# Kernel optimization log

Hardware: AMD Instinct MI355X
Metric: run time of the kernel (lower is better)

## Reference

```python
import jax, jax.numpy as jnp
import numpy as np

K = 7        # kernel_size
G = 16       # group_number
STRIDE = 1
BN_EPS = 1e-5


def setup_inputs() -> dict:
    key = jax.random.key(0)
    ks = jax.random.split(key, 3)
    B, C, H, W = 2, 256, 56, 56
    Cr = C // 4  # reduction_ratio = 4
    x = jax.random.normal(ks[0], (B, C, H, W), dtype=jnp.float32)
    w1 = jax.random.normal(ks[1], (Cr, C), dtype=jnp.float32) * (1.0 / np.sqrt(C))
    b1 = jnp.zeros((Cr,), dtype=jnp.float32)
    gamma = jnp.ones((Cr,), dtype=jnp.float32)
    beta = jnp.zeros((Cr,), dtype=jnp.float32)
    w2 = jax.random.normal(ks[2], (K * K * G, Cr), dtype=jnp.float32) * (1.0 / np.sqrt(Cr))
    b2 = jnp.zeros((K * K * G,), dtype=jnp.float32)
    return {"x": x, "w1": w1, "b1": b1, "gamma": gamma, "beta": beta, "w2": w2, "b2": b2}


def _kernel_gen(x, w1, b1, gamma, beta, w2, b2):
    # 1x1 conv -> BatchNorm (training-mode batch stats) -> ReLU -> 1x1 conv
    t = jnp.einsum('oc,bchw->bohw', w1, x) + b1[None, :, None, None]
    mean = t.mean(axis=(0, 2, 3), keepdims=True)
    var = t.var(axis=(0, 2, 3), keepdims=True)
    t = (t - mean) * jax.lax.rsqrt(var + BN_EPS)
    t = t * gamma[None, :, None, None] + beta[None, :, None, None]
    t = jax.nn.relu(t)
    return jnp.einsum('oc,bchw->bohw', w2, t) + b2[None, :, None, None]


def reference(x, w1, b1, gamma, beta, w2, b2):
    B, C, H, W = x.shape
    nh, nw = H // STRIDE, W // STRIDE  # stride == 1 here
    # kernel generation (stride==1 -> no avg_pool)
    k = _kernel_gen(x, w1, b1, gamma, beta, w2, b2)          # (B, K*K*G, nh, nw)
    kernel = k.reshape(B, K * K, nh, nw, G)                   # raw view, as in torch
    # F.unfold with padding=K//2, stride=1 -> layout (B, C*K*K, L), c-major then k
    p = K // 2
    xp = jnp.pad(x, ((0, 0), (0, 0), (p, p), (p, p)))
    patches = jnp.stack(
        [xp[:, :, i:i + nh, j:j + nw] for i in range(K) for j in range(K)],
        axis=2)                                               # (B, C, K*K, nh, nw)
    flat = patches.reshape(B, C * K * K, nh * nw)             # == torch F.unfold
    ip = flat.reshape(B, C // G, K * K, nh, nw, G)            # raw view, as in torch
    out = (kernel[:, None] * ip).sum(axis=2)                  # (B, C//G, nh, nw, G)
    out = out.reshape(B, C, nh, nw)                           # raw view, as in torch
    return out, kernel
```

## Files before the change

kernel.cpp:

```cpp
#include <hip/hip_runtime.h>

#define HW     3136
#define C_IN   256
#define CR     64
#define KKG    784
#define NB     2
#define NPIX   6272
#define NT25   25
#define BN_EPS 1e-5f

__device__ float g_P[4 * CR * NPIX];
__device__ float g_T[CR * NPIX];
__device__ float g_bs[2 * CR * NT25];
__device__ float g_xg[16 * NPIX * 16];
__device__ float g_w2t[CR * KKG];

__global__ __launch_bounds__(256) void k1a_conv1(const float* __restrict__ x,
                                                 const float* __restrict__ w1,
                                                 const float* __restrict__ w2) {
  int bid = blockIdx.x;
  if (bid >= 800) {
    int t = bid - 800;
    int idx = t * 256 + threadIdx.x;
    for (int j = idx; j < CR * KKG; j += 25 * 256) {
      int c = j / KKG, o = j - c * KKG;
      g_w2t[j] = w2[o * CR + c];
    }
    return;
  }
  int kc     = (bid & 7) >> 1;
  int parity = bid & 1;
  int unit   = (bid >> 3) * 2 + parity;
  int o0     = (unit & 7) * 8;
  int pt     = unit >> 3;
  int p      = pt * 256 + threadIdx.x;
  if (p >= NPIX) return;
  int b = p / HW;
  int u = p - b * HW;

  const float* xb = x + ((size_t)(b * C_IN + kc * 64)) * HW + u;
  const float* w  = w1 + kc * 64;

  float acc[8];
#pragma unroll
  for (int i = 0; i < 8; ++i) acc[i] = 0.0f;
#pragma unroll 8
  for (int c = 0; c < 64; ++c) {
    float xv = xb[(size_t)c * HW];
#pragma unroll
    for (int i = 0; i < 8; ++i)
      acc[i] += w[(o0 + i) * C_IN + c] * xv;
  }
  float* pp = g_P + ((size_t)kc * CR + o0) * NPIX + p;
#pragma unroll
  for (int i = 0; i < 8; ++i) pp[(size_t)i * NPIX] = acc[i];
}

__global__ __launch_bounds__(256) void kRT(const float* __restrict__ x,
                                           const float* __restrict__ b1) {
  int p = blockIdx.x * 256 + threadIdx.x;
  if (blockIdx.y < 64) {
    int o = blockIdx.y;
    bool valid = (p < NPIX);
    float v = 0.0f;
    if (valid) {
      v = b1[o]
        + g_P[((size_t)0 * CR + o) * NPIX + p]
        + g_P[((size_t)1 * CR + o) * NPIX + p]
        + g_P[((size_t)2 * CR + o) * NPIX + p]
        + g_P[((size_t)3 * CR + o) * NPIX + p];
      g_T[(size_t)o * NPIX + p] = v;
    }
    float s  = valid ? v : 0.0f;
    float s2 = valid ? v * v : 0.0f;
#pragma unroll
    for (int off = 32; off > 0; off >>= 1) {
      s  += __shfl_down(s, off);
      s2 += __shfl_down(s2, off);
    }
    __shared__ float sd[8];
    int lane = threadIdx.x & 63, wid = threadIdx.x >> 6;
    if (lane == 0) { sd[wid] = s; sd[4 + wid] = s2; }
    __syncthreads();
    if (threadIdx.x == 0) {
      g_bs[o * NT25 + blockIdx.x]             = sd[0] + sd[1] + sd[2] + sd[3];
      g_bs[CR * NT25 + o * NT25 + blockIdx.x] = sd[4] + sd[5] + sd[6] + sd[7];
    }
  } else {
    int d = blockIdx.y - 64;
    if (p >= NPIX) return;
    int b  = (p >= HW) ? 1 : 0;
    int hw = p - b * HW;
    const float* xp = x + ((size_t)(b * C_IN + d)) * HW + hw;
    float r[16];
#pragma unroll
    for (int cg = 0; cg < 16; ++cg)
      r[cg] = xp[(size_t)cg * (16 * HW)];
    float4* dst = (float4*)(g_xg + (((size_t)d * NPIX + p) << 4));
    dst[0] = make_float4(r[0], r[1], r[2], r[3]);
    dst[1] = make_float4(r[4], r[5], r[6], r[7]);
    dst[2] = make_float4(r[8], r[9], r[10], r[11]);
    dst[3] = make_float4(r[12], r[13], r[14], r[15]);
  }
}

__global__ __launch_bounds__(256) void kB_conv2(const float* __restrict__ gamma,
                                                const float* __restrict__ beta,
                                                const float* __restrict__ b2,
                                                float* __restrict__ kout) {
  __shared__ float ssc[CR], ssh[CR];
  if (threadIdx.x < CR) {
    int o = threadIdx.x;
    float S = 0.f, S2 = 0.f;
#pragma unroll
    for (int px = 0; px < NT25; ++px) {
      S  += g_bs[o * NT25 + px];
      S2 += g_bs[CR * NT25 + o * NT25 + px];
    }
    const float invN = 1.0f / (float)NPIX;
    float mean = S * invN;
    float var  = S2 * invN - mean * mean;
    float inv  = rsqrtf(var + BN_EPS);
    float sc   = gamma[o] * inv;
    ssc[o] = sc;
    ssh[o] = beta[o] - mean * sc;
  }
  __syncthreads();

  int l  = blockIdx.x * 256 + threadIdx.x;
  if (l >= HW) return;
  int o0 = blockIdx.y * 16;
  int b  = blockIdx.z;

  float acc[16];
#pragma unroll
  for (int i = 0; i < 16; ++i) acc[i] = b2[o0 + i];

  const float* Tb = g_T + (size_t)b * HW + l;
  const float* wt = g_w2t + o0;
#pragma unroll 4
  for (int c = 0; c < CR; ++c) {
    float tv = Tb[(size_t)c * NPIX];
    tv = fmaxf(tv * ssc[c] + ssh[c], 0.0f);
#pragma unroll
    for (int i = 0; i < 16; ++i)
      acc[i] += wt[c * KKG + i] * tv;
  }
  float* kb = kout + (size_t)(b * KKG + o0) * HW + l;
#pragma unroll
  for (int i = 0; i < 16; ++i) kb[(size_t)i * HW] = acc[i];
}

__global__ __launch_bounds__(256) void k4_invol(const float* __restrict__ kout,
                                                float* __restrict__ out) {
  int u = blockIdx.y * 256 + threadIdx.x;
  if (u >= HW) return;
  int s = blockIdx.x;
  int b = blockIdx.z;

  int yrow = u / 56;
  int col  = u - yrow * 56;

  const float* kb = kout + (size_t)b * (KKG * HW) + (size_t)s * HW + u;
  const size_t bHW16 = (size_t)(b * HW) << 4;

  float acc[16];
#pragma unroll
  for (int i = 0; i < 16; ++i) acc[i] = 0.0f;

#pragma unroll 7
  for (int kk = 0; kk < 49; ++kk) {
    int t16 = 16 * kk + s;
    int d   = t16 / 49;
    int kkp = t16 - d * 49;
    int ki  = kkp / 7;
    int kj  = kkp - ki * 7;
    int yy = yrow + ki - 3, xx = col + kj - 3;
    float kv = kb[(size_t)kk * (16 * HW)];
    int off;
    if ((unsigned)yy < 56u && (unsigned)xx < 56u) {
      off = yy * 56 + xx;
    } else {
      off = 0;
      kv = 0.0f;
    }
    const float* xp = g_xg + (((size_t)d * NPIX + off) << 4) + bHW16;
    float4 x0 = *(const float4*)xp;
    float4 x1 = *(const float4*)(xp + 4);
    float4 x2 = *(const float4*)(xp + 8);
    float4 x3 = *(const float4*)(xp + 12);
    acc[0]  += kv * x0.x;  acc[1]  += kv * x0.y;
    acc[2]  += kv * x0.z;  acc[3]  += kv * x0.w;
    acc[4]  += kv * x1.x;  acc[5]  += kv * x1.y;
    acc[6]  += kv * x1.z;  acc[7]  += kv * x1.w;
    acc[8]  += kv * x2.x;  acc[9]  += kv * x2.y;
    acc[10] += kv * x2.z;  acc[11] += kv * x2.w;
    acc[12] += kv * x3.x;  acc[13] += kv * x3.y;
    acc[14] += kv * x3.z;  acc[15] += kv * x3.w;
  }

  float* ob = out + (size_t)b * (C_IN * HW) + (size_t)s * HW + u;
#pragma unroll
  for (int cg = 0; cg < 16; ++cg) ob[(size_t)cg * (16 * HW)] = acc[cg];
}

extern "C" void kernel_launch(void* const* d_in, const int* in_sizes, int n_in,
                              void* d_out, int out_size, void* d_ws, size_t ws_size,
                              hipStream_t stream) {
  const float* x     = (const float*)d_in[0];
  const float* w1    = (const float*)d_in[1];
  const float* b1    = (const float*)d_in[2];
  const float* gamma = (const float*)d_in[3];
  const float* beta  = (const float*)d_in[4];
  const float* w2    = (const float*)d_in[5];
  const float* b2    = (const float*)d_in[6];

  float* out  = (float*)d_out;
  float* kout = out + (size_t)NB * C_IN * HW;

  k1a_conv1<<<dim3(825), 256, 0, stream>>>(x, w1, w2);
  kRT<<<dim3(25, 80), 256, 0, stream>>>(x, b1);
  kB_conv2<<<dim3(13, 49, NB), 256, 0, stream>>>(gamma, beta, b2, kout);
  k4_invol<<<dim3(16, 13, NB), 256, 0, stream>>>(kout, out);
}
```

Baseline: 124.1 us.

## Fuse conv1, bias, BN partial stats and x regroup into one kernel

Merges the split-K conv1 kernel and the reduce/stats/regroup kernel into a single launch. Each block now runs the full 256-channel reduction for 8 output channels, adds the bias, writes T directly and computes per-tile BN sum and sum-of-squares partials, so the g_P partial buffer and one kernel launch go away. The x regroup and w2 transpose run as extra block ranges in the same grid, with a remapped block order. The trade-off is fewer conv1 blocks (200) each doing 4x longer loops, which lowers parallelism and latency hiding for that phase.

```diff
diff --git a/kernel.cpp b/kernel.cpp
--- a/kernel.cpp
+++ b/kernel.cpp
@@ -9,18 +9,18 @@
 #define NT25   25
 #define BN_EPS 1e-5f
 
-__device__ float g_P[4 * CR * NPIX];
 __device__ float g_T[CR * NPIX];
 __device__ float g_bs[2 * CR * NT25];
 __device__ float g_xg[16 * NPIX * 16];
 __device__ float g_w2t[CR * KKG];
 
-__global__ __launch_bounds__(256) void k1a_conv1(const float* __restrict__ x,
-                                                 const float* __restrict__ w1,
-                                                 const float* __restrict__ w2) {
+__global__ __launch_bounds__(256) void k1f(const float* __restrict__ x,
+                                           const float* __restrict__ w1,
+                                           const float* __restrict__ b1,
+                                           const float* __restrict__ w2) {
   int bid = blockIdx.x;
-  if (bid >= 800) {
-    int t = bid - 800;
+  if (bid >= 600) {
+    int t = bid - 600;
     int idx = t * 256 + threadIdx.x;
     for (int j = idx; j < CR * KKG; j += 25 * 256) {
       int c = j / KKG, o = j - c * KKG;
@@ -28,66 +28,12 @@
     }
     return;
   }
-  int kc     = (bid & 7) >> 1;
-  int parity = bid & 1;
-  int unit   = (bid >> 3) * 2 + parity;
-  int o0     = (unit & 7) * 8;
-  int pt     = unit >> 3;
-  int p      = pt * 256 + threadIdx.x;
-  if (p >= NPIX) return;
-  int b = p / HW;
-  int u = p - b * HW;
-
-  const float* xb = x + ((size_t)(b * C_IN + kc * 64)) * HW + u;
-  const float* w  = w1 + kc * 64;
-
-  float acc[8];
-#pragma unroll
-  for (int i = 0; i < 8; ++i) acc[i] = 0.0f;
-#pragma unroll 8
-  for (int c = 0; c < 64; ++c) {
-    float xv = xb[(size_t)c * HW];
-#pragma unroll
-    for (int i = 0; i < 8; ++i)
-      acc[i] += w[(o0 + i) * C_IN + c] * xv;
-  }
-  float* pp = g_P + ((size_t)kc * CR + o0) * NPIX + p;
-#pragma unroll
-  for (int i = 0; i < 8; ++i) pp[(size_t)i * NPIX] = acc[i];
-}
-
-__global__ __launch_bounds__(256) void kRT(const float* __restrict__ x,
-                                           const float* __restrict__ b1) {
-  int p = blockIdx.x * 256 + threadIdx.x;
-  if (blockIdx.y < 64) {
-    int o = blockIdx.y;
-    bool valid = (p < NPIX);
-    float v = 0.0f;
-    if (valid) {
-      v = b1[o]
-        + g_P[((size_t)0 * CR + o) * NPIX + p]
-        + g_P[((size_t)1 * CR + o) * NPIX + p]
-        + g_P[((size_t)2 * CR + o) * NPIX + p]
-        + g_P[((size_t)3 * CR + o) * NPIX + p];
-      g_T[(size_t)o * NPIX + p] = v;
-    }
-    float s  = valid ? v : 0.0f;
-    float s2 = valid ? v * v : 0.0f;
-#pragma unroll
-    for (int off = 32; off > 0; off >>= 1) {
-      s  += __shfl_down(s, off);
-      s2 += __shfl_down(s2, off);
-    }
-    __shared__ float sd[8];
-    int lane = threadIdx.x & 63, wid = threadIdx.x >> 6;
-    if (lane == 0) { sd[wid] = s; sd[4 + wid] = s2; }
-    __syncthreads();
-    if (threadIdx.x == 0) {
-      g_bs[o * NT25 + blockIdx.x]             = sd[0] + sd[1] + sd[2] + sd[3];
-      g_bs[CR * NT25 + o * NT25 + blockIdx.x] = sd[4] + sd[5] + sd[6] + sd[7];
-    }
-  } else {
-    int d = blockIdx.y - 64;
+  if (bid >= 200) {
+    int t  = bid - 200;
+    int g  = (t & 7) * 50 + (t >> 3);
+    int pt = g >> 4;
+    int d  = g & 15;
+    int p  = pt * 256 + threadIdx.x;
     if (p >= NPIX) return;
     int b  = (p >= HW) ? 1 : 0;
     int hw = p - b * HW;
@@ -101,6 +47,55 @@
     dst[1] = make_float4(r[4], r[5], r[6], r[7]);
     dst[2] = make_float4(r[8], r[9], r[10], r[11]);
     dst[3] = make_float4(r[12], r[13], r[14], r[15]);
+    return;
+  }
+  int unit = (bid & 7) * 25 + (bid >> 3);
+  int pt   = unit >> 3;
+  int o0   = (unit & 7) * 8;
+  int p    = pt * 256 + threadIdx.x;
+  bool valid = (p < NPIX);
+  int pc   = valid ? p : 0;
+  int b    = pc / HW;
+  int u    = pc - b * HW;
+
+  const float* xb = x + (size_t)(b * C_IN) * HW + u;
+
+  float acc[8];
+#pragma unroll
+  for (int i = 0; i < 8; ++i) acc[i] = b1[o0 + i];
+#pragma unroll 8
+  for (int c = 0; c < C_IN; ++c) {
+    float xv = xb[(size_t)c * HW];
+#pragma unroll
+    for (int i = 0; i < 8; ++i)
+      acc[i] += w1[(o0 + i) * C_IN + c] * xv;
+  }
+  if (valid) {
+    float* pp = g_T + (size_t)o0 * NPIX + p;
+#pragma unroll
+    for (int i = 0; i < 8; ++i) pp[(size_t)i * NPIX] = acc[i];
+  }
+  __shared__ float red[16][4];
+  int lane = threadIdx.x & 63, wid = threadIdx.x >> 6;
+#pragma unroll
+  for (int i = 0; i < 8; ++i) {
+    float s  = valid ? acc[i] : 0.0f;
+    float s2 = s * s;
+#pragma unroll
+    for (int off = 32; off > 0; off >>= 1) {
+      s  += __shfl_down(s, off);
+      s2 += __shfl_down(s2, off);
+    }
+    if (lane == 0) { red[i][wid] = s; red[8 + i][wid] = s2; }
+  }
+  __syncthreads();
+  if (threadIdx.x < 8) {
+    int i = threadIdx.x;
+    g_bs[(o0 + i) * NT25 + pt] = red[i][0] + red[i][1] + red[i][2] + red[i][3];
+  } else if (threadIdx.x < 16) {
+    int i = threadIdx.x - 8;
+    g_bs[CR * NT25 + (o0 + i) * NT25 + pt] =
+        red[8 + i][0] + red[8 + i][1] + red[8 + i][2] + red[8 + i][3];
   }
 }
 
@@ -218,8 +213,7 @@
   float* out  = (float*)d_out;
   float* kout = out + (size_t)NB * C_IN * HW;
 
-  k1a_conv1<<<dim3(825), 256, 0, stream>>>(x, w1, w2);
-  kRT<<<dim3(25, 80), 256, 0, stream>>>(x, b1);
+  k1f<<<dim3(625), 256, 0, stream>>>(x, w1, b1, w2);
   kB_conv2<<<dim3(13, 49, NB), 256, 0, stream>>>(gamma, beta, b2, kout);
   k4_invol<<<dim3(16, 13, NB), 256, 0, stream>>>(kout, out);
 }
```

Result: slower. 132.8 us (+7.0%).

## Fuse conv2 kernel generation into involution kernel, keeping activations in registers

Applied to the files above, without the earlier changes.

Merges the second 1x1 conv (BN+ReLU+conv2) into the involution kernel. Each thread loads its 64 normalized activations into registers, computes each kernel weight on the fly with a 64-term dot product, writes it to kout, and uses it right away, so kout is no longer read back from global memory and one launch is removed. The w2 weights are pre-permuted into a per-s layout so they can be read as uniform, broadcastable values. The cost is more register pressure (64 activation registers plus 16 accumulators) and a small grid of 416 blocks doing all the conv2 FLOPs, which may lower occupancy.

```diff
diff --git a/kernel.cpp b/kernel.cpp
--- a/kernel.cpp
+++ b/kernel.cpp
@@ -13,7 +13,7 @@
 __device__ float g_T[CR * NPIX];
 __device__ float g_bs[2 * CR * NT25];
 __device__ float g_xg[16 * NPIX * 16];
-__device__ float g_w2t[CR * KKG];
+__device__ float g_w2s[16 * 49 * CR];
 
 __global__ __launch_bounds__(256) void k1a_conv1(const float* __restrict__ x,
                                                  const float* __restrict__ w1,
@@ -22,9 +22,12 @@
   if (bid >= 800) {
     int t = bid - 800;
     int idx = t * 256 + threadIdx.x;
-    for (int j = idx; j < CR * KKG; j += 25 * 256) {
-      int c = j / KKG, o = j - c * KKG;
-      g_w2t[j] = w2[o * CR + c];
+    for (int j = idx; j < 16 * 49 * CR; j += 25 * 256) {
+      int s  = j / 3136;
+      int r  = j - s * 3136;
+      int kk = r >> 6;
+      int c  = r & 63;
+      g_w2s[j] = w2[(16 * kk + s) * CR + c];
     }
     return;
   }
@@ -104,10 +107,11 @@
   }
 }
 
-__global__ __launch_bounds__(256) void kB_conv2(const float* __restrict__ gamma,
-                                                const float* __restrict__ beta,
-                                                const float* __restrict__ b2,
-                                                float* __restrict__ kout) {
+__global__ __launch_bounds__(256) void k45(const float* __restrict__ gamma,
+                                           const float* __restrict__ beta,
+                                           const float* __restrict__ b2,
+                                           float* __restrict__ kout,
+                                           float* __restrict__ out) {
   __shared__ float ssc[CR], ssh[CR];
   if (threadIdx.x < CR) {
     int o = threadIdx.x;
@@ -127,42 +131,22 @@
   }
   __syncthreads();
 
-  int l  = blockIdx.x * 256 + threadIdx.x;
-  if (l >= HW) return;
-  int o0 = blockIdx.y * 16;
-  int b  = blockIdx.z;
-
-  float acc[16];
-#pragma unroll
-  for (int i = 0; i < 16; ++i) acc[i] = b2[o0 + i];
-
-  const float* Tb = g_T + (size_t)b * HW + l;
-  const float* wt = g_w2t + o0;
-#pragma unroll 4
-  for (int c = 0; c < CR; ++c) {
-    float tv = Tb[(size_t)c * NPIX];
-    tv = fmaxf(tv * ssc[c] + ssh[c], 0.0f);
-#pragma unroll
-    for (int i = 0; i < 16; ++i)
-      acc[i] += wt[c * KKG + i] * tv;
-  }
-  float* kb = kout + (size_t)(b * KKG + o0) * HW + l;
-#pragma unroll
-  for (int i = 0; i < 16; ++i) kb[(size_t)i * HW] = acc[i];
-}
-
-__global__ __launch_bounds__(256) void k4_invol(const float* __restrict__ kout,
-                                                float* __restrict__ out) {
   int u = blockIdx.y * 256 + threadIdx.x;
   if (u >= HW) return;
   int s = blockIdx.x;
   int b = blockIdx.z;
 
+  float t_reg[CR];
+  const float* Tb = g_T + (size_t)b * HW + u;
+#pragma unroll
+  for (int c = 0; c < CR; ++c)
+    t_reg[c] = fmaxf(fmaf(Tb[(size_t)c * NPIX], ssc[c], ssh[c]), 0.0f);
+
   int yrow = u / 56;
   int col  = u - yrow * 56;
-
-  const float* kb = kout + (size_t)b * (KKG * HW) + (size_t)s * HW + u;
   const size_t bHW16 = (size_t)(b * HW) << 4;
+  float* kb = kout + (size_t)b * (KKG * HW) + (size_t)s * HW + u;
+  const float* wbase = g_w2s + (size_t)s * (49 * CR);
 
   float acc[16];
 #pragma unroll
@@ -170,13 +154,24 @@
 
 #pragma unroll 7
   for (int kk = 0; kk < 49; ++kk) {
+    const float* wrow = wbase + kk * CR;
+    float kv0 = 0.f, kv1 = 0.f, kv2 = 0.f, kv3 = 0.f;
+#pragma unroll
+    for (int c = 0; c < CR; c += 4) {
+      kv0 = fmaf(wrow[c + 0], t_reg[c + 0], kv0);
+      kv1 = fmaf(wrow[c + 1], t_reg[c + 1], kv1);
+      kv2 = fmaf(wrow[c + 2], t_reg[c + 2], kv2);
+      kv3 = fmaf(wrow[c + 3], t_reg[c + 3], kv3);
+    }
     int t16 = 16 * kk + s;
+    float kv = b2[t16] + ((kv0 + kv1) + (kv2 + kv3));
+    kb[(size_t)kk * (16 * HW)] = kv;
+
     int d   = t16 / 49;
     int kkp = t16 - d * 49;
     int ki  = kkp / 7;
     int kj  = kkp - ki * 7;
     int yy = yrow + ki - 3, xx = col + kj - 3;
-    float kv = kb[(size_t)kk * (16 * HW)];
     int off;
     if ((unsigned)yy < 56u && (unsigned)xx < 56u) {
       off = yy * 56 + xx;
@@ -220,6 +215,5 @@
 
   k1a_conv1<<<dim3(825), 256, 0, stream>>>(x, w1, w2);
   kRT<<<dim3(25, 80), 256, 0, stream>>>(x, b1);
-  kB_conv2<<<dim3(13, 49, NB), 256, 0, stream>>>(gamma, beta, b2, kout);
-  k4_invol<<<dim3(16, 13, NB), 256, 0, stream>>>(kout, out);
-}
+  k45<<<dim3(16, 13, NB), 256, 0, stream>>>(gamma, beta, b2, kout, out);
+}
```

After: 127.3 us. +2.6%, slower.
